# Kernel optimization log

Measured on AMD Instinct MI355X. Metric: run time of the kernel, lower is better.

Reference implementation:

```python
import jax, jax.numpy as jnp
import numpy as np

N = 100000
E = 3200000
C = 32
EPS = 1e-5
SLOPE = 0.01  # nn.LeakyReLU default negative slope


def _param_key(i):
    return jax.random.fold_in(jax.random.key(42), i)


def setup_inputs() -> dict:
    key = jax.random.key(0)
    k0, k1, k2, k3 = jax.random.split(key, 4)
    patch_embs = jax.random.normal(k0, (N, C), jnp.float32)
    row = jax.random.randint(k1, (E,), 0, N)
    off = jax.random.randint(k2, (E,), 1, N)
    col = (row + off) % N  # guarantees no self loops (PyG removes+re-adds them)
    edge_index = jnp.stack([row, col]).astype(jnp.int64)
    edge_attr = jax.random.normal(k3, (E, 1), jnp.float32)
    s = 1.0 / np.sqrt(C)
    inp = {"patch_embs": patch_embs, "edge_index": edge_index, "edge_attr": edge_attr}
    for i in (1, 2, 3):
        ka, kb = jax.random.split(_param_key(i))
        inp[f"W{i}_out"] = jax.random.uniform(ka, (C, C), jnp.float32, -s, s)
        inp[f"b{i}_out"] = jnp.zeros((C,), jnp.float32)
        inp[f"W{i}_root"] = jax.random.uniform(kb, (C, C), jnp.float32, -s, s)
        inp[f"g{i}"] = jnp.ones((C,), jnp.float32)
        inp[f"be{i}"] = jnp.zeros((C,), jnp.float32)
    return inp


def _cluster_gcn(x, row, col, W_out, b_out, W_root):
    n = x.shape[0]
    loops = jnp.arange(n, dtype=row.dtype)
    r = jnp.concatenate([row, loops])
    c = jnp.concatenate([col, loops])
    deg = jax.ops.segment_sum(jnp.ones_like(c, jnp.float32), c, num_segments=n)
    deg_inv = 1.0 / jnp.clip(deg, 1.0)  # degree(col).clamp_(1.)
    w = deg_inv[c]  # diag_lambda = 0 default
    agg = jax.ops.segment_sum(x[r] * w[:, None], c, num_segments=n)
    return agg @ W_out + b_out + x @ W_root


def _bn_train(x, g, b):
    m = jnp.mean(x, axis=0)
    v = jnp.mean(jnp.square(x - m), axis=0)  # biased var, BatchNorm1d training
    return (x - m) * jax.lax.rsqrt(v + EPS) * g + b


def _leaky(x):
    return jnp.where(x >= 0, x, SLOPE * x)


def reference(patch_embs, edge_index, edge_attr,
              W1_out, b1_out, W1_root, g1, be1,
              W2_out, b2_out, W2_root, g2, be2,
              W3_out, b3_out, W3_root, g3, be3):
    row, col = edge_index[0], edge_index[1]
    x = _bn_train(_leaky(_cluster_gcn(patch_embs, row, col, W1_out, b1_out, W1_root)) + patch_embs, g1, be1)
    x = _bn_train(_leaky(_cluster_gcn(x, row, col, W2_out, b2_out, W2_root)) + x, g2, be2)
    x = _bn_train(_cluster_gcn(x, row, col, W3_out, b3_out, W3_root) + x, g3, be3)
    return x
```

## Files before the change

### kernel.cpp

```cpp
#include <hip/hip_runtime.h>
#include <hip/hip_fp8.h>

#define SLOPE 0.01f
#define BN_EPS 1e-5f
#define CH 32
#define GATHER_BLOCKS 6250
#define DENSE_BLOCKS 2048
#define APPLY_BLOCKS 1024

#define BSH 8
#define BNODES 256
#define NBMAX 512

#if defined(__has_builtin)
#if __has_builtin(__builtin_amdgcn_cvt_pk_f32_fp8)
#define USE_CVT_PK 1
#endif
#endif

typedef float v2f __attribute__((ext_vector_type(2)));
typedef float v4f __attribute__((ext_vector_type(4)));

static __device__ __forceinline__ float q2f(unsigned char b) {
    __hip_fp8_e4m3 t;
    t.__x = (__hip_fp8_storage_t)b;
    return (float)t;
}
static __device__ __forceinline__ unsigned char f2q(float f) {
    __hip_fp8_e4m3 t(f);
    return (unsigned char)t.__x;
}
static __device__ __forceinline__ unsigned short f2bf(float f) {
    unsigned int x = __float_as_uint(f);
    x += 0x7fffu + ((x >> 16) & 1u);
    return (unsigned short)(x >> 16);
}
static __device__ __forceinline__ float bf2f(unsigned int u16) {
    return __uint_as_float(u16 << 16);
}
static __device__ __forceinline__ void dec_add(unsigned int u, float4& a) {
#ifdef USE_CVT_PK
    v2f lo = __builtin_amdgcn_cvt_pk_f32_fp8((int)u, false);
    v2f hi = __builtin_amdgcn_cvt_pk_f32_fp8((int)u, true);
    a.x += lo.x; a.y += lo.y; a.z += hi.x; a.w += hi.y;
#else
    a.x += q2f((unsigned char)(u & 0xff));
    a.y += q2f((unsigned char)((u >> 8) & 0xff));
    a.z += q2f((unsigned char)((u >> 16) & 0xff));
    a.w += q2f((unsigned char)(u >> 24));
#endif
}
static __device__ __forceinline__ void nt_store4(const float4& a, float4* p) {
    v4f t; t.x = a.x; t.y = a.y; t.z = a.z; t.w = a.w;
    __builtin_nontemporal_store(t, (v4f*)p);
}


__global__ __launch_bounds__(256) void hist_kernel(const int* __restrict__ col,
        int* __restrict__ ghist, int nE, int nb) {
    __shared__ int h[NBMAX];
    for (int i = threadIdx.x; i < nb; i += 256) h[i] = 0;
    __syncthreads();
    for (int e = blockIdx.x * 256 + threadIdx.x; e < nE; e += gridDim.x * 256)
        atomicAdd(&h[col[e] >> BSH], 1);
    __syncthreads();
    for (int i = threadIdx.x; i < nb; i += 256) {
        int v = h[i];
        if (v) atomicAdd(&ghist[i], v);
    }
}

__global__ __launch_bounds__(512) void bscan_kernel(const int* __restrict__ ghist,
        int* __restrict__ bbase, int* __restrict__ gcur, int nb,
        int* __restrict__ off, int n) {
    __shared__ int sh[512];
    int tid = threadIdx.x;
    int v = (tid < nb) ? ghist[tid] : 0;
    sh[tid] = v;
    __syncthreads();
    int acc = v;
#pragma unroll
    for (int d = 1; d < 512; d <<= 1) {
        int t = (tid >= d) ? sh[tid - d] : 0;
        __syncthreads();
        acc += t;
        sh[tid] = acc;
        __syncthreads();
    }
    int excl = acc - v;
    if (tid < nb) { bbase[tid] = excl; gcur[tid] = excl; }
    if (tid == nb - 1) { bbase[nb] = acc; off[n] = acc; }
}

__global__ __launch_bounds__(1024) void part_kernel(const int* __restrict__ row,
        const int* __restrict__ col, int* __restrict__ gcur,
        unsigned int* __restrict__ staging, int nE, int nb) {
    __shared__ int hist[NBMAX], gb[NBMAX], lcur[NBMAX];
    int tid = threadIdx.x;
    for (int i = tid; i < nb; i += 1024) hist[i] = 0;
    __syncthreads();
    int base = blockIdx.x * 8192;
    int r[8], bk[8];
    unsigned int lo[8];
    bool ok[8];
#pragma unroll
    for (int k = 0; k < 8; ++k) {
        int e = base + (k << 10) + tid;
        ok[k] = (e < nE);
        if (ok[k]) {
            int rr = row[e], cc = col[e];
            r[k] = rr; bk[k] = cc >> BSH; lo[k] = (unsigned)(cc & (BNODES - 1));
            atomicAdd(&hist[bk[k]], 1);
        }
    }
    __syncthreads();
    for (int i = tid; i < nb; i += 1024) {
        int h = hist[i];
        if (h) gb[i] = atomicAdd(&gcur[i], h);
        lcur[i] = 0;
    }
    __syncthreads();
#pragma unroll
    for (int k = 0; k < 8; ++k) {
        if (ok[k]) {
            int b = bk[k];
            int p = gb[b] + atomicAdd(&lcur[b], 1);
            staging[p] = ((unsigned)r[k] << BSH) | lo[k];
        }
    }
}

__global__ __launch_bounds__(256) void build_kernel(const unsigned int* __restrict__ staging,
        const int* __restrict__ bbase, int* __restrict__ adj, int* __restrict__ off,
        float* __restrict__ dinv, int n) {
    int b = blockIdx.x;
    int b0 = b << BSH;
    int tid = threadIdx.x;
    int es = bbase[b], ee = bbase[b + 1];
    __shared__ int cnt[BNODES];
    __shared__ int bs[BNODES];
    __shared__ int wsum[4], woff[4];
    cnt[tid] = 0;
    __syncthreads();
    for (int i = es + tid; i < ee; i += 256)
        atomicAdd(&cnt[staging[i] & (BNODES - 1)], 1);
    __syncthreads();
    int v = cnt[tid];
    int lane = tid & 63, wid = tid >> 6;
    int xs = v;
#pragma unroll
    for (int d = 1; d < 64; d <<= 1) {
        int t = __shfl_up(xs, d, 64);
        if (lane >= d) xs += t;
    }
    if (lane == 63) wsum[wid] = xs;
    __syncthreads();
    if (tid == 0) {
        int run = 0;
#pragma unroll
        for (int k = 0; k < 4; ++k) { woff[k] = run; run += wsum[k]; }
    }
    __syncthreads();
    bs[tid] = xs - v + woff[wid];
    int node = b0 + tid;
    if (node < n) {
        off[node] = es + bs[tid];
        dinv[node] = 1.0f / (float)(v + 1);
    }
    __syncthreads();
    for (int i = es + tid; i < ee; i += 256) {
        unsigned int w = staging[i];
        int c = w & (BNODES - 1);
        int p = atomicAdd(&bs[c], 1);
        adj[es + p] = (int)(w >> BSH);
    }
}


__global__ __launch_bounds__(256) void cast_kernel(const float4* __restrict__ x4,
        unsigned int* __restrict__ xq4, int n4) {
    for (int i = blockIdx.x * blockDim.x + threadIdx.x; i < n4; i += gridDim.x * blockDim.x) {
        float4 v = x4[i];
        unsigned int o = (unsigned int)f2q(v.x)
                       | ((unsigned int)f2q(v.y) << 8)
                       | ((unsigned int)f2q(v.z) << 16)
                       | ((unsigned int)f2q(v.w) << 24);
        xq4[i] = o;
    }
}


__global__ __launch_bounds__(256, 8) void gather_kernel(
        const unsigned char* __restrict__ xq,
        const int* __restrict__ off, const int* __restrict__ adj,
        float4* __restrict__ S4, int n) {
    int tid = threadIdx.x;
    int lane = tid & 63, w = tid >> 6;
    int h = lane >> 5;
    int q = (lane & 31) >> 2;
    int r = lane & 3;
    int half0 = (blockIdx.x * 4 + w) * 2 + h;
    int nH = gridDim.x * 8;
    for (int p = half0; 2 * p < n; p += nH) {
        int v0 = 2 * p, v1 = v0 + 1;
        int s0 = off[v0], e0 = off[v0 + 1];
        int s1 = 0, e1 = 0;
        if (v1 < n) { s1 = off[v1]; e1 = off[v1 + 1]; }
        float4 a0A = {0.f,0.f,0.f,0.f}, a0B = {0.f,0.f,0.f,0.f};
        float4 a1A = {0.f,0.f,0.f,0.f}, a1B = {0.f,0.f,0.f,0.f};
        int j0 = s0, j1 = s1;
        while (j0 + 15 < e0 && j1 + 15 < e1) {
            int i00 = adj[j0 + q],     i01 = adj[j0 + 8 + q];
            int i10 = adj[j1 + q],     i11 = adj[j1 + 8 + q];
            uint2 u00 = *(const uint2*)(xq + (size_t)i00 * CH + r * 8);
            uint2 u01 = *(const uint2*)(xq + (size_t)i01 * CH + r * 8);
            uint2 u10 = *(const uint2*)(xq + (size_t)i10 * CH + r * 8);
            uint2 u11 = *(const uint2*)(xq + (size_t)i11 * CH + r * 8);
            dec_add(u00.x, a0A); dec_add(u00.y, a0B);
            dec_add(u01.x, a0A); dec_add(u01.y, a0B);
            dec_add(u10.x, a1A); dec_add(u10.y, a1B);
            dec_add(u11.x, a1A); dec_add(u11.y, a1B);
            j0 += 16; j1 += 16;
        }
        for (; j0 + 7 < e0; j0 += 8) {
            int i0 = adj[j0 + q];
            uint2 u = *(const uint2*)(xq + (size_t)i0 * CH + r * 8);
            dec_add(u.x, a0A); dec_add(u.y, a0B);
        }
        if (j0 < e0) {
            int jj = j0 + q;
            if (jj < e0) {
                uint2 u = *(const uint2*)(xq + (size_t)adj[jj] * CH + r * 8);
                dec_add(u.x, a0A); dec_add(u.y, a0B);
            }
        }
        for (; j1 + 7 < e1; j1 += 8) {
            int i0 = adj[j1 + q];
            uint2 u = *(const uint2*)(xq + (size_t)i0 * CH + r * 8);
            dec_add(u.x, a1A); dec_add(u.y, a1B);
        }
        if (j1 < e1) {
            int jj = j1 + q;
            if (jj < e1) {
                uint2 u = *(const uint2*)(xq + (size_t)adj[jj] * CH + r * 8);
                dec_add(u.x, a1A); dec_add(u.y, a1B);
            }
        }
#define MRG4(a, m) a.x += __shfl_xor(a.x, m); a.y += __shfl_xor(a.y, m); \
                   a.z += __shfl_xor(a.z, m); a.w += __shfl_xor(a.w, m);
        MRG4(a0A, 4)  MRG4(a0B, 4)  MRG4(a1A, 4)  MRG4(a1B, 4)
        MRG4(a0A, 8)  MRG4(a0B, 8)  MRG4(a1A, 8)  MRG4(a1B, 8)
        MRG4(a0A, 16) MRG4(a0B, 16) MRG4(a1A, 16) MRG4(a1B, 16)
#undef MRG4
        if (q == 0) {
            nt_store4(a0A, &S4[(size_t)v0 * 8 + r * 2]);
            nt_store4(a0B, &S4[(size_t)v0 * 8 + r * 2 + 1]);
            if (v1 < n) {
                nt_store4(a1A, &S4[(size_t)v1 * 8 + r * 2]);
                nt_store4(a1B, &S4[(size_t)v1 * 8 + r * 2 + 1]);
            }
        }
    }
}


__global__ __launch_bounds__(256) void dense_kernel(
        const float* __restrict__ x, float* __restrict__ Sz,
        const float* __restrict__ dinv,
        const float* __restrict__ Wout, const float* __restrict__ bout,
        const float* __restrict__ Wroot,
        float* __restrict__ partials, int n, int do_leaky) {
    __shared__ float2 WI[CH * CH];
    __shared__ float red[2][4][CH];
    int tid = threadIdx.x;
    for (int i = tid; i < CH * CH; i += 256)
        WI[i] = make_float2(Wout[i], Wroot[i]);
    __syncthreads();
    int lane = tid & 63, w = tid >> 6;
    int c = lane & 31, h = lane >> 5;
    float bo = bout[c];
    int hw0 = (blockIdx.x * 4 + w) * 2 + h;
    int nHW = gridDim.x * 8;
    float bsum = 0.f, bsq = 0.f;
    for (int v = hw0; v < n; v += nHW) {
        float Sv = Sz[(size_t)v * CH + c];
        float xv = x[(size_t)v * CH + c];
        float a = (Sv + xv) * dinv[v];
        unsigned int pk = (unsigned int)f2bf(a) | ((unsigned int)f2bf(xv) << 16);
        float2 acc0 = {0.f, 0.f}, acc1 = {0.f, 0.f};
        float2 acc2 = {0.f, 0.f}, acc3 = {0.f, 0.f};
#pragma unroll
        for (int k = 0; k < CH; k += 4) {
            unsigned int p0 = __shfl(pk, k,     32);
            unsigned int p1 = __shfl(pk, k + 1, 32);
            unsigned int p2 = __shfl(pk, k + 2, 32);
            unsigned int p3 = __shfl(pk, k + 3, 32);
            float2 w0 = WI[k * CH + c];
            float2 w1 = WI[(k + 1) * CH + c];
            float2 w2 = WI[(k + 2) * CH + c];
            float2 w3 = WI[(k + 3) * CH + c];
            acc0.x += bf2f(p0 & 0xffffu) * w0.x; acc0.y += bf2f(p0 >> 16) * w0.y;
            acc1.x += bf2f(p1 & 0xffffu) * w1.x; acc1.y += bf2f(p1 >> 16) * w1.y;
            acc2.x += bf2f(p2 & 0xffffu) * w2.x; acc2.y += bf2f(p2 >> 16) * w2.y;
            acc3.x += bf2f(p3 & 0xffffu) * w3.x; acc3.y += bf2f(p3 >> 16) * w3.y;
        }
        float y = ((acc0.x + acc0.y) + (acc1.x + acc1.y))
                + ((acc2.x + acc2.y) + (acc3.x + acc3.y)) + bo;
        float zz = do_leaky ? (y >= 0.f ? y : SLOPE * y) : y;
        zz += xv;
        Sz[(size_t)v * CH + c] = zz;
        bsum += zz; bsq += zz * zz;
    }
    bsum += __shfl_xor(bsum, 32);
    bsq  += __shfl_xor(bsq, 32);
    if (h == 0) { red[0][w][c] = bsum; red[1][w][c] = bsq; }
    __syncthreads();
    if (tid < 64) {
        int which = tid >> 5, cc = tid & 31;
        float sv = red[which][0][cc] + red[which][1][cc] + red[which][2][cc] + red[which][3][cc];
        partials[blockIdx.x * 64 + which * 32 + cc] = sv;
    }
}


__global__ __launch_bounds__(1024) void finalizeA_kernel(const float* __restrict__ partials,
        float* __restrict__ parts2, int nblk) {
    int tid = threadIdx.x;
    int col = tid & 63, grp = tid >> 6;
    int rows = nblk >> 6;
    int r0 = blockIdx.x * rows;
    float s = 0.f;
    for (int r = grp; r < rows; r += 16) s += partials[(r0 + r) * 64 + col];
    __shared__ float red[16][64];
    red[grp][col] = s;
    __syncthreads();
    if (tid < 64) {
        float tot = 0.f;
#pragma unroll
        for (int k = 0; k < 16; ++k) tot += red[k][tid];
        parts2[blockIdx.x * 64 + tid] = tot;
    }
}

__global__ __launch_bounds__(1024) void finalizeB_kernel(const float* __restrict__ parts2,
        const float* __restrict__ g, const float* __restrict__ be,
        float* __restrict__ st, int n) {
    int tid = threadIdx.x;
    int col = tid & 63, grp = tid >> 6;
    double s = 0.0;
    for (int r = grp; r < 64; r += 16) s += (double)parts2[r * 64 + col];
    __shared__ double red[16][64];
    red[grp][col] = s;
    __syncthreads();
    if (tid < 64) {
        double tot = 0.0;
#pragma unroll
        for (int k = 0; k < 16; ++k) tot += red[k][tid];
        red[0][tid] = tot;
    }
    __syncthreads();
    if (tid < 32) {
        double mean = red[0][tid] / (double)n;
        double var = red[0][32 + tid] / (double)n - mean * mean;
        float inv = rsqrtf(fmaxf((float)var, 0.f) + BN_EPS);
        float sc = (float)(g[tid] * inv);
        st[tid] = sc;
        st[32 + tid] = be[tid] - (float)mean * sc;
    }
}

__global__ __launch_bounds__(256) void bn_apply_kernel(const float4* __restrict__ z4,
        const float* __restrict__ st, float4* __restrict__ xout,
        unsigned int* __restrict__ xq4, int n4, int write_q) {
    __shared__ float sL[64];
    if (threadIdx.x < 64) sL[threadIdx.x] = st[threadIdx.x];
    __syncthreads();
    for (int i = blockIdx.x * blockDim.x + threadIdx.x; i < n4; i += gridDim.x * blockDim.x) {
        float4 zz = z4[i];
        int c0 = (i & 7) * 4;
        float4 o;
        o.x = zz.x * sL[c0]     + sL[32 + c0];
        o.y = zz.y * sL[c0 + 1] + sL[32 + c0 + 1];
        o.z = zz.z * sL[c0 + 2] + sL[32 + c0 + 2];
        o.w = zz.w * sL[c0 + 3] + sL[32 + c0 + 3];
        xout[i] = o;
        if (write_q) {
            unsigned int oq = (unsigned int)f2q(o.x)
                            | ((unsigned int)f2q(o.y) << 8)
                            | ((unsigned int)f2q(o.z) << 16)
                            | ((unsigned int)f2q(o.w) << 24);
            xq4[i] = oq;
        }
    }
}


extern "C" void kernel_launch(void* const* d_in, const int* in_sizes, int n_in,
                              void* d_out, int out_size, void* d_ws, size_t ws_size,
                              hipStream_t stream) {
    const float* x0 = (const float*)d_in[0];
    const int* ei = (const int*)d_in[1];
    int nE = in_sizes[1] / 2;
    int n = in_sizes[0] / CH;
    const int* row = ei;
    const int* col = ei + nE;
    const float* W_out[3]  = {(const float*)d_in[3],  (const float*)d_in[8],  (const float*)d_in[13]};
    const float* b_out[3]  = {(const float*)d_in[4],  (const float*)d_in[9],  (const float*)d_in[14]};
    const float* W_root[3] = {(const float*)d_in[5],  (const float*)d_in[10], (const float*)d_in[15]};
    const float* gam[3]    = {(const float*)d_in[6],  (const float*)d_in[11], (const float*)d_in[16]};
    const float* bet[3]    = {(const float*)d_in[7],  (const float*)d_in[12], (const float*)d_in[17]};

    int nb = (n + BNODES - 1) >> BSH;

    char* w = (char*)d_ws;
    auto carve = [&](size_t bytes) { char* p = w; w += (bytes + 511) & ~511ull; return p; };
    int*   off     = (int*)  carve((size_t)(n + 1) * 4);
    int*   adj     = (int*)  carve((size_t)nE * 4);
    float* dinv    = (float*)carve((size_t)n * 4);
    int*   ghist   = (int*)  carve((size_t)NBMAX * 4);
    int*   bbase   = (int*)  carve((size_t)(NBMAX + 1) * 4);
    int*   gcur    = (int*)  carve((size_t)NBMAX * 4);
    size_t zbytes  = (size_t)n * CH * 4;
    size_t sbytes  = (size_t)nE * 4;
    char*  uni     = (char*) carve(zbytes > sbytes ? zbytes : sbytes);
    unsigned int* staging = (unsigned int*)uni;
    float* Sz      = (float*)uni;
    float* xbuf    = (float*)carve(zbytes);
    unsigned char* xq = (unsigned char*)carve((size_t)n * CH);
    float* parts   = (float*)carve((size_t)GATHER_BLOCKS * 64 * 4);
    float* parts2  = (float*)carve((size_t)64 * 64 * 4);
    float* st      = (float*)carve(256);

    hipMemsetAsync(ghist, 0, (size_t)NBMAX * 4, stream);
    hist_kernel<<<1024, 256, 0, stream>>>(col, ghist, nE, nb);
    bscan_kernel<<<1, 512, 0, stream>>>(ghist, bbase, gcur, nb, off, n);
    int pb = (nE + 8191) / 8192;
    part_kernel<<<pb, 1024, 0, stream>>>(row, col, gcur, staging, nE, nb);
    build_kernel<<<nb, 256, 0, stream>>>(staging, bbase, adj, off, dinv, n);

    int n4 = n * CH / 4;
    cast_kernel<<<APPLY_BLOCKS, 256, 0, stream>>>((const float4*)x0, (unsigned int*)xq, n4);

    const float* xin = x0;
    for (int L = 0; L < 3; ++L) {
        float* xout = (L == 2) ? (float*)d_out : xbuf;
        gather_kernel<<<GATHER_BLOCKS, 256, 0, stream>>>(xq, off, adj, (float4*)Sz, n);
        dense_kernel<<<DENSE_BLOCKS, 256, 0, stream>>>(xin, Sz, dinv,
                W_out[L], b_out[L], W_root[L], parts, n, (L < 2) ? 1 : 0);
        finalizeA_kernel<<<64, 1024, 0, stream>>>(parts, parts2, DENSE_BLOCKS);
        finalizeB_kernel<<<1, 1024, 0, stream>>>(parts2, gam[L], bet[L], st, n);
        bn_apply_kernel<<<APPLY_BLOCKS, 256, 0, stream>>>((const float4*)Sz, st,
                (float4*)xout, (unsigned int*)xq, n4, (L < 2) ? 1 : 0);
        xin = xout;
    }
}
```

Measured before the change: 289.2 us.

## Fold BatchNorm apply into next layer's dense kernel and fuse finalize into gather

The BatchNorm scale and shift are no longer applied in a separate pass between layers. The next layer's dense kernel applies them algebraically to the pre-BN activations and to the aggregated neighbor sum, which is exact because the mean aggregation weights sum to one. The dense kernel now writes the fp8 quantized copy directly. The two-stage BN statistic finalize is folded into an extra block of the gather kernel, and the initial cast is fused into the histogram kernel. This removes two full-tensor read/write passes and several small launches, at the cost of quantizing pre-normalization values to fp8 (a different dynamic range) and of fewer dense blocks.

```diff
diff --git a/kernel.cpp b/kernel.cpp
--- a/kernel.cpp
+++ b/kernel.cpp
@@ -5,7 +5,7 @@
 #define BN_EPS 1e-5f
 #define CH 32
 #define GATHER_BLOCKS 6250
-#define DENSE_BLOCKS 2048
+#define DENSE_BLOCKS 1024
 #define APPLY_BLOCKS 1024
 
 #define BSH 8
@@ -55,14 +55,63 @@
     __builtin_nontemporal_store(t, (v4f*)p);
 }
 
-
-__global__ __launch_bounds__(256) void hist_kernel(const int* __restrict__ col,
-        int* __restrict__ ghist, int nE, int nb) {
+static __device__ __forceinline__ void fin_body(const float* __restrict__ partials,
+        int nprt, const float* __restrict__ g, const float* __restrict__ be,
+        float* __restrict__ stO, int nv) {
+    __shared__ float4 red4[16][16];
+    __shared__ double sdv[64];
+    int tid = threadIdx.x;
+    const float4* p4 = (const float4*)partials;
+    int col4 = tid & 15, grp = tid >> 4;
+    float4 s = make_float4(0.f, 0.f, 0.f, 0.f);
+    for (int r = grp; r < nprt; r += 16) {
+        float4 t = p4[(size_t)r * 16 + col4];
+        s.x += t.x; s.y += t.y; s.z += t.z; s.w += t.w;
+    }
+    red4[grp][col4] = s;
+    __syncthreads();
+    if (tid < 64) {
+        int c4 = tid >> 2, cc = tid & 3;
+        double tot = 0.0;
+#pragma unroll
+        for (int k = 0; k < 16; ++k) {
+            const float* rr = (const float*)&red4[k][c4];
+            tot += (double)rr[cc];
+        }
+        sdv[tid] = tot;
+    }
+    __syncthreads();
+    if (tid < 32) {
+        double mean = sdv[tid] / (double)nv;
+        double var  = sdv[32 + tid] / (double)nv - mean * mean;
+        float inv = rsqrtf(fmaxf((float)var, 0.f) + BN_EPS);
+        float scv = g[tid] * inv;
+        stO[tid] = scv;
+        stO[32 + tid] = be[tid] - (float)mean * scv;
+    }
+}
+
+
+__global__ __launch_bounds__(256) void cast_hist_kernel(
+        const float4* __restrict__ x4, unsigned int* __restrict__ xq4, int n4,
+        const int* __restrict__ col, int* __restrict__ ghist, int nE, int nb,
+        float* __restrict__ st0) {
     __shared__ int h[NBMAX];
     for (int i = threadIdx.x; i < nb; i += 256) h[i] = 0;
     __syncthreads();
-    for (int e = blockIdx.x * 256 + threadIdx.x; e < nE; e += gridDim.x * 256)
+    int gt = blockIdx.x * 256 + threadIdx.x, gs = gridDim.x * 256;
+    for (int e = gt; e < nE; e += gs)
         atomicAdd(&h[col[e] >> BSH], 1);
+    for (int i = gt; i < n4; i += gs) {
+        float4 v = x4[i];
+        unsigned int o = (unsigned int)f2q(v.x)
+                       | ((unsigned int)f2q(v.y) << 8)
+                       | ((unsigned int)f2q(v.z) << 16)
+                       | ((unsigned int)f2q(v.w) << 24);
+        xq4[i] = o;
+    }
+    if (blockIdx.x == 0 && threadIdx.x < 64)
+        st0[threadIdx.x] = (threadIdx.x < 32) ? 1.0f : 0.0f;
     __syncthreads();
     for (int i = threadIdx.x; i < nb; i += 256) {
         int v = h[i];
@@ -177,30 +226,24 @@
 }
 
 
-__global__ __launch_bounds__(256) void cast_kernel(const float4* __restrict__ x4,
-        unsigned int* __restrict__ xq4, int n4) {
-    for (int i = blockIdx.x * blockDim.x + threadIdx.x; i < n4; i += gridDim.x * blockDim.x) {
-        float4 v = x4[i];
-        unsigned int o = (unsigned int)f2q(v.x)
-                       | ((unsigned int)f2q(v.y) << 8)
-                       | ((unsigned int)f2q(v.z) << 16)
-                       | ((unsigned int)f2q(v.w) << 24);
-        xq4[i] = o;
-    }
-}
-
-
 __global__ __launch_bounds__(256, 8) void gather_kernel(
         const unsigned char* __restrict__ xq,
         const int* __restrict__ off, const int* __restrict__ adj,
-        float4* __restrict__ S4, int n) {
+        float4* __restrict__ S4, int n,
+        const float* __restrict__ partials, int nprt,
+        const float* __restrict__ g, const float* __restrict__ be,
+        float* __restrict__ st_out) {
+    if (blockIdx.x >= GATHER_BLOCKS) {
+        if (partials) fin_body(partials, nprt, g, be, st_out, n);
+        return;
+    }
     int tid = threadIdx.x;
     int lane = tid & 63, w = tid >> 6;
     int h = lane >> 5;
     int q = (lane & 31) >> 2;
     int r = lane & 3;
     int half0 = (blockIdx.x * 4 + w) * 2 + h;
-    int nH = gridDim.x * 8;
+    int nH = GATHER_BLOCKS * 8;
     for (int p = half0; 2 * p < n; p += nH) {
         int v0 = 2 * p, v1 = v0 + 1;
         int s0 = off[v0], e0 = off[v0 + 1];
@@ -265,11 +308,12 @@
 
 
 __global__ __launch_bounds__(256) void dense_kernel(
-        const float* __restrict__ x, float* __restrict__ Sz,
-        const float* __restrict__ dinv,
+        const float* __restrict__ zin, float* __restrict__ Sz,
+        const float* __restrict__ dinv, const float* __restrict__ st,
         const float* __restrict__ Wout, const float* __restrict__ bout,
         const float* __restrict__ Wroot,
-        float* __restrict__ partials, int n, int do_leaky) {
+        float* __restrict__ partials, unsigned int* __restrict__ zq4,
+        int n, int do_leaky) {
     __shared__ float2 WI[CH * CH];
     __shared__ float red[2][4][CH];
     int tid = threadIdx.x;
@@ -279,13 +323,15 @@
     int lane = tid & 63, w = tid >> 6;
     int c = lane & 31, h = lane >> 5;
     float bo = bout[c];
+    float sc = st[c], sh = st[32 + c];
     int hw0 = (blockIdx.x * 4 + w) * 2 + h;
     int nHW = gridDim.x * 8;
     float bsum = 0.f, bsq = 0.f;
     for (int v = hw0; v < n; v += nHW) {
         float Sv = Sz[(size_t)v * CH + c];
-        float xv = x[(size_t)v * CH + c];
-        float a = (Sv + xv) * dinv[v];
+        float zv = zin[(size_t)v * CH + c];
+        float xv = fmaf(sc, zv, sh);
+        float a = fmaf(sc * (Sv + zv), dinv[v], sh);
         unsigned int pk = (unsigned int)f2bf(a) | ((unsigned int)f2bf(xv) << 16);
         float2 acc0 = {0.f, 0.f}, acc1 = {0.f, 0.f};
         float2 acc2 = {0.f, 0.f}, acc3 = {0.f, 0.f};
@@ -310,6 +356,14 @@
         zz += xv;
         Sz[(size_t)v * CH + c] = zz;
         bsum += zz; bsq += zz * zz;
+        if (zq4) {
+            unsigned int b0 = (unsigned int)f2q(zz);
+            unsigned int b1 = __shfl_down(b0, 1, 32);
+            unsigned int b2 = __shfl_down(b0, 2, 32);
+            unsigned int b3 = __shfl_down(b0, 3, 32);
+            if ((c & 3) == 0)
+                zq4[(size_t)v * 8 + (c >> 2)] = b0 | (b1 << 8) | (b2 << 16) | (b3 << 24);
+        }
     }
     bsum += __shfl_xor(bsum, 32);
     bsq  += __shfl_xor(bsq, 32);
@@ -323,55 +377,14 @@
 }
 
 
-__global__ __launch_bounds__(1024) void finalizeA_kernel(const float* __restrict__ partials,
-        float* __restrict__ parts2, int nblk) {
-    int tid = threadIdx.x;
-    int col = tid & 63, grp = tid >> 6;
-    int rows = nblk >> 6;
-    int r0 = blockIdx.x * rows;
-    float s = 0.f;
-    for (int r = grp; r < rows; r += 16) s += partials[(r0 + r) * 64 + col];
-    __shared__ float red[16][64];
-    red[grp][col] = s;
-    __syncthreads();
-    if (tid < 64) {
-        float tot = 0.f;
-#pragma unroll
-        for (int k = 0; k < 16; ++k) tot += red[k][tid];
-        parts2[blockIdx.x * 64 + tid] = tot;
-    }
-}
-
-__global__ __launch_bounds__(1024) void finalizeB_kernel(const float* __restrict__ parts2,
-        const float* __restrict__ g, const float* __restrict__ be,
-        float* __restrict__ st, int n) {
-    int tid = threadIdx.x;
-    int col = tid & 63, grp = tid >> 6;
-    double s = 0.0;
-    for (int r = grp; r < 64; r += 16) s += (double)parts2[r * 64 + col];
-    __shared__ double red[16][64];
-    red[grp][col] = s;
-    __syncthreads();
-    if (tid < 64) {
-        double tot = 0.0;
-#pragma unroll
-        for (int k = 0; k < 16; ++k) tot += red[k][tid];
-        red[0][tid] = tot;
-    }
-    __syncthreads();
-    if (tid < 32) {
-        double mean = red[0][tid] / (double)n;
-        double var = red[0][32 + tid] / (double)n - mean * mean;
-        float inv = rsqrtf(fmaxf((float)var, 0.f) + BN_EPS);
-        float sc = (float)(g[tid] * inv);
-        st[tid] = sc;
-        st[32 + tid] = be[tid] - (float)mean * sc;
-    }
+__global__ __launch_bounds__(256) void fin_kernel(const float* __restrict__ partials,
+        int nprt, const float* __restrict__ g, const float* __restrict__ be,
+        float* __restrict__ stO, int nv) {
+    fin_body(partials, nprt, g, be, stO, nv);
 }
 
 __global__ __launch_bounds__(256) void bn_apply_kernel(const float4* __restrict__ z4,
-        const float* __restrict__ st, float4* __restrict__ xout,
-        unsigned int* __restrict__ xq4, int n4, int write_q) {
+        const float* __restrict__ st, float4* __restrict__ xout, int n4) {
     __shared__ float sL[64];
     if (threadIdx.x < 64) sL[threadIdx.x] = st[threadIdx.x];
     __syncthreads();
@@ -384,13 +397,6 @@
         o.z = zz.z * sL[c0 + 2] + sL[32 + c0 + 2];
         o.w = zz.w * sL[c0 + 3] + sL[32 + c0 + 3];
         xout[i] = o;
-        if (write_q) {
-            unsigned int oq = (unsigned int)f2q(o.x)
-                            | ((unsigned int)f2q(o.y) << 8)
-                            | ((unsigned int)f2q(o.z) << 16)
-                            | ((unsigned int)f2q(o.w) << 24);
-            xq4[i] = oq;
-        }
     }
 }
 
@@ -424,33 +430,34 @@
     size_t sbytes  = (size_t)nE * 4;
     char*  uni     = (char*) carve(zbytes > sbytes ? zbytes : sbytes);
     unsigned int* staging = (unsigned int*)uni;
-    float* Sz      = (float*)uni;
-    float* xbuf    = (float*)carve(zbytes);
+    float* bufA    = (float*)uni;
+    float* bufB    = (float*)carve(zbytes);
     unsigned char* xq = (unsigned char*)carve((size_t)n * CH);
-    float* parts   = (float*)carve((size_t)GATHER_BLOCKS * 64 * 4);
-    float* parts2  = (float*)carve((size_t)64 * 64 * 4);
-    float* st      = (float*)carve(256);
+    float* parts   = (float*)carve((size_t)DENSE_BLOCKS * 64 * 4);
+    float* stb     = (float*)carve((size_t)4 * 64 * 4);
 
     hipMemsetAsync(ghist, 0, (size_t)NBMAX * 4, stream);
-    hist_kernel<<<1024, 256, 0, stream>>>(col, ghist, nE, nb);
+    int n4 = n * CH / 4;
+    cast_hist_kernel<<<1024, 256, 0, stream>>>((const float4*)x0, (unsigned int*)xq, n4,
+            col, ghist, nE, nb, stb);
     bscan_kernel<<<1, 512, 0, stream>>>(ghist, bbase, gcur, nb, off, n);
     int pb = (nE + 8191) / 8192;
     part_kernel<<<pb, 1024, 0, stream>>>(row, col, gcur, staging, nE, nb);
     build_kernel<<<nb, 256, 0, stream>>>(staging, bbase, adj, off, dinv, n);
 
-    int n4 = n * CH / 4;
-    cast_kernel<<<APPLY_BLOCKS, 256, 0, stream>>>((const float4*)x0, (unsigned int*)xq, n4);
-
-    const float* xin = x0;
-    for (int L = 0; L < 3; ++L) {
-        float* xout = (L == 2) ? (float*)d_out : xbuf;
-        gather_kernel<<<GATHER_BLOCKS, 256, 0, stream>>>(xq, off, adj, (float4*)Sz, n);
-        dense_kernel<<<DENSE_BLOCKS, 256, 0, stream>>>(xin, Sz, dinv,
-                W_out[L], b_out[L], W_root[L], parts, n, (L < 2) ? 1 : 0);
-        finalizeA_kernel<<<64, 1024, 0, stream>>>(parts, parts2, DENSE_BLOCKS);
-        finalizeB_kernel<<<1, 1024, 0, stream>>>(parts2, gam[L], bet[L], st, n);
-        bn_apply_kernel<<<APPLY_BLOCKS, 256, 0, stream>>>((const float4*)Sz, st,
-                (float4*)xout, (unsigned int*)xq, n4, (L < 2) ? 1 : 0);
-        xin = xout;
-    }
-}
+    gather_kernel<<<GATHER_BLOCKS + 1, 256, 0, stream>>>(xq, off, adj, (float4*)bufA, n,
+            nullptr, 0, nullptr, nullptr, nullptr);
+    dense_kernel<<<DENSE_BLOCKS, 256, 0, stream>>>(x0, bufA, dinv, stb,
+            W_out[0], b_out[0], W_root[0], parts, (unsigned int*)xq, n, 1);
+    gather_kernel<<<GATHER_BLOCKS + 1, 256, 0, stream>>>(xq, off, adj, (float4*)bufB, n,
+            parts, DENSE_BLOCKS, gam[0], bet[0], stb + 64);
+    dense_kernel<<<DENSE_BLOCKS, 256, 0, stream>>>(bufA, bufB, dinv, stb + 64,
+            W_out[1], b_out[1], W_root[1], parts, (unsigned int*)xq, n, 1);
+    gather_kernel<<<GATHER_BLOCKS + 1, 256, 0, stream>>>(xq, off, adj, (float4*)bufA, n,
+            parts, DENSE_BLOCKS, gam[1], bet[1], stb + 128);
+    dense_kernel<<<DENSE_BLOCKS, 256, 0, stream>>>(bufB, bufA, dinv, stb + 128,
+            W_out[2], b_out[2], W_root[2], parts, nullptr, n, 0);
+    fin_kernel<<<1, 256, 0, stream>>>(parts, DENSE_BLOCKS, gam[2], bet[2], stb + 192, n);
+    bn_apply_kernel<<<APPLY_BLOCKS, 256, 0, stream>>>((const float4*)bufA, stb + 192,
+            (float4*)d_out, n4);
+}
```

Measured after the change: 303.4 us. 1.05x slower.
